# Kernel optimization log

Hardware: AMD Instinct MI355X
Metric: run time of the kernel (lower is better)

## Reference

```python
import jax, jax.numpy as jnp
import numpy as np

MAX_OUTPUT = 25
SHARPNESS = 10.0

def soft_clamp(x, min_val, max_val, sharpness=SHARPNESS):
    x_norm = (x - min_val) / (max_val - min_val + 1e-06)
    x_clamped = jax.nn.sigmoid(sharpness * (x_norm - 0.5))
    return min_val + x_clamped * (max_val - min_val)

def setup_inputs() -> dict:
    key = jax.random.key(0)
    k1, = jax.random.split(key, 1)
    T = 2_000_000
    input_seq = jax.random.randint(k1, (T,), 0, 2, dtype=jnp.int32)
    # learned parameters, matching torch init values
    delta = jnp.array([0.5, -0.5], dtype=jnp.float32)
    out_scale = jnp.array(5.0, dtype=jnp.float32)
    return {"delta": delta, "out_scale": out_scale, "input_seq": input_seq}

def reference(delta, out_scale, input_seq):
    # counter_t = sum_{i<=t} delta[input_seq[i]]  (clamped value is NOT fed back,
    # so the recurrence is an exact cumulative sum)
    steps = delta[input_seq]                       # [T]
    counter = jnp.cumsum(steps)                    # [T]
    counter_soft = soft_clamp(counter, 0.0, float(MAX_OUTPUT - 1))  # [T]
    positions = jnp.arange(MAX_OUTPUT, dtype=counter_soft.dtype)    # [25]
    distances = jnp.abs(positions[None, :] - counter_soft[:, None]) # [T, 25]
    logits = -distances * out_scale
    return jax.nn.softmax(logits, axis=-1)         # [T, 25]
```

## Files before the change

### kernel.cpp

```cpp
#include <hip/hip_runtime.h>
#include <hip/hip_bf16.h>

#define MAXO 25
#define CHUNK 512

__global__ __launch_bounds__(256) void pda_pass1(
    const int* __restrict__ seq, unsigned* __restrict__ chunk_sums,
    int T, int nchunks)
{
    const int lane = threadIdx.x & 63;
    const int wid  = threadIdx.x >> 6;
    const int chunk = blockIdx.x * 4 + wid;
    if (chunk >= nchunks) return;

    const long base = (long)chunk * CHUNK;
    unsigned sum = 0;
    #pragma unroll
    for (int r = 0; r < 8; ++r) {
        long t = base + (long)r * 64 + lane;
        int b = (t < (long)T) ? seq[t] : 0;
        unsigned long long m = __ballot(b != 0);
        sum += (unsigned)__popcll(m);
    }
    if (lane == 0) chunk_sums[chunk] = sum;
}

__global__ __launch_bounds__(1024) void pda_scan(unsigned* __restrict__ buf, int n)
{
    __shared__ unsigned wsum[16];
    __shared__ unsigned carry;
    const int lane = threadIdx.x & 63;
    const int wid  = threadIdx.x >> 6;
    if (threadIdx.x == 0) carry = 0;
    __syncthreads();

    for (int base = 0; base < n; base += 1024) {
        int i = base + (int)threadIdx.x;
        unsigned v = (i < n) ? buf[i] : 0u;

        unsigned x = v;
        #pragma unroll
        for (int off = 1; off < 64; off <<= 1) {
            unsigned y = __shfl_up(x, off, 64);
            if (lane >= off) x += y;
        }
        if (lane == 63) wsum[wid] = x;
        __syncthreads();

        if (wid == 0) {
            unsigned w = (lane < 16) ? wsum[lane] : 0u;
            #pragma unroll
            for (int off = 1; off < 16; off <<= 1) {
                unsigned y = __shfl_up(w, off, 64);
                if (lane >= off) w += y;
            }
            if (lane < 16) wsum[lane] = w;
        }
        __syncthreads();

        unsigned wexcl = wid ? wsum[wid - 1] : 0u;
        unsigned total = wsum[15];
        unsigned myc   = carry;
        unsigned excl  = myc + wexcl + (x - v);
        if (i < n) buf[i] = excl;
        __syncthreads();
        if (threadIdx.x == 0) carry = myc + total;
        __syncthreads();
    }
}

__global__ __launch_bounds__(256) void pda_main(
    const int* __restrict__ seq, const unsigned* __restrict__ chunk_excl,
    const float* __restrict__ delta, const float* __restrict__ scale_p,
    float* __restrict__ out, int T, int nchunks)
{
    __shared__ __align__(16) float stage[4][64 * MAXO];

    const int lane = threadIdx.x & 63;
    const int wid  = threadIdx.x >> 6;
    const int chunk = blockIdx.x * 4 + wid;
    const bool active = (chunk < nchunks);

    const float d0 = delta[0];
    const float dd = delta[1] - d0;
    const float scale = scale_p[0];
    const float inv_denom = 1.0f / (24.0f + 1e-6f);

    const long cbase = (long)chunk * CHUNK;
    unsigned run = active ? chunk_excl[chunk] : 0u;
    const unsigned long long le_mask = (lane == 63) ? ~0ULL : ((2ULL << lane) - 1ULL);

    for (int r = 0; r < 8; ++r) {
        const long rbase = cbase + (long)r * 64;
        const long t = rbase + lane;
        const bool tv = active && (t < (long)T);

        int b = tv ? seq[t] : 0;
        unsigned long long m = __ballot(b != 0);
        unsigned ones_incl = run + (unsigned)__popcll(m & le_mask);

        float c  = (float)(t + 1) * d0 + (float)ones_incl * dd;
        float z  = 10.0f * (c * inv_denom - 0.5f);
        float sig = 1.0f / (1.0f + __expf(-z));
        float cs = sig * 24.0f;

        float w[MAXO];
        float sum = 0.0f;
        #pragma unroll
        for (int j = 0; j < MAXO; ++j) {
            float dist = fabsf((float)j - cs);
            w[j] = __expf(-scale * dist);
            sum += w[j];
        }
        float inv = 1.0f / sum;

        __syncthreads();
        #pragma unroll
        for (int j = 0; j < MAXO; ++j)
            stage[wid][lane * MAXO + j] = w[j] * inv;
        __syncthreads();

        int V = 0;
        if (active) {
            long rem = (long)T - rbase;
            V = (rem >= 64) ? 64 : (rem < 0 ? 0 : (int)rem);
        }

        if (V == 64) {
            float4* o4 = (float4*)(out + rbase * MAXO);
            const float4* s4 = (const float4*)&stage[wid][0];
            #pragma unroll
            for (int s = 0; s < 6; ++s)
                o4[s * 64 + lane] = s4[s * 64 + lane];
            if (lane < 16) o4[384 + lane] = s4[384 + lane];
        } else if (V > 0) {
            int F = V * MAXO;
            for (int f = lane; f < F; f += 64)
                out[rbase * MAXO + f] = stage[wid][f];
        }

        run += (unsigned)__popcll(m);
    }
}

extern "C" void kernel_launch(void* const* d_in, const int* in_sizes, int n_in,
                              void* d_out, int out_size, void* d_ws, size_t ws_size,
                              hipStream_t stream)
{
    const float* delta   = (const float*)d_in[0];
    const float* scale_p = (const float*)d_in[1];
    const int*   seq     = (const int*)d_in[2];
    const int T = in_sizes[2];
    const int nchunks = (T + CHUNK - 1) / CHUNK;

    unsigned* ws1 = (unsigned*)d_ws;

    const int blocks = (nchunks + 3) / 4;
    pda_pass1<<<blocks, 256, 0, stream>>>(seq, ws1, T, nchunks);
    pda_scan <<<1, 1024, 0, stream>>>(ws1, nchunks);
    pda_main <<<blocks, 256, 0, stream>>>(seq, ws1, delta, scale_p,
                                          (float*)d_out, T, nchunks);
}
```

Measured before the change: 48.27 us.

## Replace single-block scan with per-block prefix reduction of block sums

Removes the serial single-block scan kernel; each main-kernel block now reduces the sums of all preceding blocks itself and combines per-wave counts in shared memory. The sums kernel uses vectorized int4 loads and adds raw values, which assumes inputs are 0/1. This trades a launch and a serialized pass for redundant quadratic-ish reads of block sums from L2.

```diff
diff --git a/kernel.cpp b/kernel.cpp
--- a/kernel.cpp
+++ b/kernel.cpp
@@ -2,107 +2,88 @@
 #include <hip/hip_bf16.h>
 
 #define MAXO 25
-#define CHUNK 512
+#define WCHUNK 512
+#define BCHUNK 2048
 
-__global__ __launch_bounds__(256) void pda_pass1(
-    const int* __restrict__ seq, unsigned* __restrict__ chunk_sums,
-    int T, int nchunks)
+__global__ __launch_bounds__(256) void pda_sums(
+    const int* __restrict__ seq, unsigned* __restrict__ blk_sums, int T)
 {
+    __shared__ unsigned ws[4];
     const int lane = threadIdx.x & 63;
     const int wid  = threadIdx.x >> 6;
-    const int chunk = blockIdx.x * 4 + wid;
-    if (chunk >= nchunks) return;
 
-    const long base = (long)chunk * CHUNK;
-    unsigned sum = 0;
+    const long t0 = (long)blockIdx.x * BCHUNK + (long)wid * WCHUNK + (long)lane * 8;
+    unsigned s = 0;
+    if (t0 + 8 <= (long)T) {
+        const int4* p = (const int4*)(seq + t0);
+        int4 a = p[0], b = p[1];
+        s = (unsigned)(a.x + a.y + a.z + a.w + b.x + b.y + b.z + b.w);
+    } else {
+        for (int k = 0; k < 8; ++k) {
+            long t = t0 + k;
+            if (t < (long)T) s += (unsigned)seq[t];
+        }
+    }
     #pragma unroll
-    for (int r = 0; r < 8; ++r) {
-        long t = base + (long)r * 64 + lane;
-        int b = (t < (long)T) ? seq[t] : 0;
-        unsigned long long m = __ballot(b != 0);
-        sum += (unsigned)__popcll(m);
-    }
-    if (lane == 0) chunk_sums[chunk] = sum;
-}
-
-__global__ __launch_bounds__(1024) void pda_scan(unsigned* __restrict__ buf, int n)
-{
-    __shared__ unsigned wsum[16];
-    __shared__ unsigned carry;
-    const int lane = threadIdx.x & 63;
-    const int wid  = threadIdx.x >> 6;
-    if (threadIdx.x == 0) carry = 0;
+    for (int off = 32; off; off >>= 1) s += __shfl_down(s, off, 64);
+    if (lane == 0) ws[wid] = s;
     __syncthreads();
-
-    for (int base = 0; base < n; base += 1024) {
-        int i = base + (int)threadIdx.x;
-        unsigned v = (i < n) ? buf[i] : 0u;
-
-        unsigned x = v;
-        #pragma unroll
-        for (int off = 1; off < 64; off <<= 1) {
-            unsigned y = __shfl_up(x, off, 64);
-            if (lane >= off) x += y;
-        }
-        if (lane == 63) wsum[wid] = x;
-        __syncthreads();
-
-        if (wid == 0) {
-            unsigned w = (lane < 16) ? wsum[lane] : 0u;
-            #pragma unroll
-            for (int off = 1; off < 16; off <<= 1) {
-                unsigned y = __shfl_up(w, off, 64);
-                if (lane >= off) w += y;
-            }
-            if (lane < 16) wsum[lane] = w;
-        }
-        __syncthreads();
-
-        unsigned wexcl = wid ? wsum[wid - 1] : 0u;
-        unsigned total = wsum[15];
-        unsigned myc   = carry;
-        unsigned excl  = myc + wexcl + (x - v);
-        if (i < n) buf[i] = excl;
-        __syncthreads();
-        if (threadIdx.x == 0) carry = myc + total;
-        __syncthreads();
-    }
+    if (threadIdx.x == 0)
+        blk_sums[blockIdx.x] = ws[0] + ws[1] + ws[2] + ws[3];
 }
 
 __global__ __launch_bounds__(256) void pda_main(
-    const int* __restrict__ seq, const unsigned* __restrict__ chunk_excl,
+    const int* __restrict__ seq, const unsigned* __restrict__ blk_sums,
     const float* __restrict__ delta, const float* __restrict__ scale_p,
-    float* __restrict__ out, int T, int nchunks)
+    float* __restrict__ out, int T)
 {
     __shared__ __align__(16) float stage[4][64 * MAXO];
+    __shared__ unsigned wsum[4];
+    __shared__ unsigned bpart[4];
 
     const int lane = threadIdx.x & 63;
     const int wid  = threadIdx.x >> 6;
-    const int chunk = blockIdx.x * 4 + wid;
-    const bool active = (chunk < nchunks);
+    const int bid  = blockIdx.x;
+    const long wbase = (long)bid * BCHUNK + (long)wid * WCHUNK;
 
     const float d0 = delta[0];
     const float dd = delta[1] - d0;
     const float scale = scale_p[0];
     const float inv_denom = 1.0f / (24.0f + 1e-6f);
 
-    const long cbase = (long)chunk * CHUNK;
-    unsigned run = active ? chunk_excl[chunk] : 0u;
+    unsigned long long m[8];
+    unsigned mycnt = 0;
+    #pragma unroll
+    for (int r = 0; r < 8; ++r) {
+        long t = wbase + (long)r * 64 + lane;
+        int b = (t < (long)T) ? seq[t] : 0;
+        m[r] = __ballot(b != 0);
+        mycnt += (unsigned)__popcll(m[r]);
+    }
+    if (lane == 0) wsum[wid] = mycnt;
+
+    unsigned p = 0;
+    for (int i = (int)threadIdx.x; i < bid; i += 256) p += blk_sums[i];
+    #pragma unroll
+    for (int off = 32; off; off >>= 1) p += __shfl_down(p, off, 64);
+    if (lane == 0) bpart[wid] = p;
+    __syncthreads();
+
+    unsigned run = bpart[0] + bpart[1] + bpart[2] + bpart[3];
+    for (int w = 0; w < wid; ++w) run += wsum[w];
+
     const unsigned long long le_mask = (lane == 63) ? ~0ULL : ((2ULL << lane) - 1ULL);
 
     for (int r = 0; r < 8; ++r) {
-        const long rbase = cbase + (long)r * 64;
+        const long rbase = wbase + (long)r * 64;
         const long t = rbase + lane;
-        const bool tv = active && (t < (long)T);
 
-        int b = tv ? seq[t] : 0;
-        unsigned long long m = __ballot(b != 0);
-        unsigned ones_incl = run + (unsigned)__popcll(m & le_mask);
+        unsigned ones_incl = run + (unsigned)__popcll(m[r] & le_mask);
 
-        float c  = (float)(t + 1) * d0 + (float)ones_incl * dd;
-        float z  = 10.0f * (c * inv_denom - 0.5f);
+        float c   = (float)(t + 1) * d0 + (float)ones_incl * dd;
+        float z   = 10.0f * (c * inv_denom - 0.5f);
         float sig = 1.0f / (1.0f + __expf(-z));
-        float cs = sig * 24.0f;
+        float cs  = sig * 24.0f;
 
         float w[MAXO];
         float sum = 0.0f;
@@ -120,11 +101,8 @@
             stage[wid][lane * MAXO + j] = w[j] * inv;
         __syncthreads();
 
-        int V = 0;
-        if (active) {
-            long rem = (long)T - rbase;
-            V = (rem >= 64) ? 64 : (rem < 0 ? 0 : (int)rem);
-        }
+        long rem = (long)T - rbase;
+        int V = (rem >= 64) ? 64 : (rem < 0 ? 0 : (int)rem);
 
         if (V == 64) {
             float4* o4 = (float4*)(out + rbase * MAXO);
@@ -139,7 +117,7 @@
                 out[rbase * MAXO + f] = stage[wid][f];
         }
 
-        run += (unsigned)__popcll(m);
+        run += (unsigned)__popcll(m[r]);
     }
 }
 
@@ -151,13 +129,11 @@
     const float* scale_p = (const float*)d_in[1];
     const int*   seq     = (const int*)d_in[2];
     const int T = in_sizes[2];
-    const int nchunks = (T + CHUNK - 1) / CHUNK;
+    const int nblocks = (T + BCHUNK - 1) / BCHUNK;
 
-    unsigned* ws1 = (unsigned*)d_ws;
+    unsigned* blk_sums = (unsigned*)d_ws;
 
-    const int blocks = (nchunks + 3) / 4;
-    pda_pass1<<<blocks, 256, 0, stream>>>(seq, ws1, T, nchunks);
-    pda_scan <<<1, 1024, 0, stream>>>(ws1, nchunks);
-    pda_main <<<blocks, 256, 0, stream>>>(seq, ws1, delta, scale_p,
-                                          (float*)d_out, T, nchunks);
+    pda_sums<<<nblocks, 256, 0, stream>>>(seq, blk_sums, T);
+    pda_main<<<nblocks, 256, 0, stream>>>(seq, blk_sums, delta, scale_p,
+                                          (float*)d_out, T);
 }
```

Measured after the change: 43.11 us. 10.7% less time.
